# Optimization experiments

Hardware: AMD Instinct MI355X
Metric: run time of the kernel (lower is better)

Reference implementation:

```python
import jax, jax.numpy as jnp
import numpy as np

B, N, HID, H, DH, NB = 4, 4096, 768, 12, 64, 266
EPS = 1e-4


def softmax_kernel(data, proj, is_query):
    # data: [B,H,N,DH], proj: [NB,DH]. FAVOR+ positive softmax features.
    d = data.shape[-1]
    ratio = proj.shape[0] ** -0.5
    dn = d ** -0.25  # data normalizer
    data_dash = jnp.einsum('bhnd,jd->bhnj', data * dn, proj)  # [B,H,N,NB]
    diag = 0.5 * jnp.sum((data * dn) ** 2, axis=-1, keepdims=True)  # [B,H,N,1]
    if is_query:
        m = jnp.max(data_dash, axis=-1, keepdims=True)
    else:
        m = jnp.max(data_dash, axis=(-1, -2), keepdims=True)
    return ratio * (jnp.exp(data_dash - diag - m) + EPS)


def setup_inputs() -> dict:
    key = jax.random.key(0)
    ks = jax.random.split(key, 8)
    s = HID ** -0.5
    return {
        'hidden_states': jax.random.normal(ks[0], (B, N, HID), jnp.float32),
        'Wq': jax.random.normal(ks[1], (HID, HID), jnp.float32) * s,
        'bq': jnp.zeros((HID,), jnp.float32),
        'Wk': jax.random.normal(ks[2], (HID, HID), jnp.float32) * s,
        'bk': jnp.zeros((HID,), jnp.float32),
        'Wv': jax.random.normal(ks[3], (HID, HID), jnp.float32) * s,
        'bv': jnp.zeros((HID,), jnp.float32),
        'proj': jax.random.normal(ks[4], (NB, DH), jnp.float32),
    }


def reference(hidden_states, Wq, bq, Wk, bk, Wv, bv, proj):
    def heads(x):  # [B,N,HID] -> [B,H,N,DH]
        return x.reshape(B, N, H, DH).transpose(0, 2, 1, 3)

    q = heads(hidden_states @ Wq.T + bq)
    k = heads(hidden_states @ Wk.T + bk)
    v = heads(hidden_states @ Wv.T + bv)

    qp = softmax_kernel(q, proj, True)   # [B,H,N,NB]
    kp = softmax_kernel(k, proj, False)  # [B,H,N,NB]

    # non-causal linear attention: out = q' (k'^T v) / (q' sum_n k')
    k_sum = jnp.sum(kp, axis=2)                               # [B,H,NB]
    d_inv = 1.0 / jnp.einsum('bhnj,bhj->bhn', qp, k_sum)      # [B,H,N]
    ctx = jnp.einsum('bhnj,bhnd->bhjd', kp, v)                # [B,H,NB,DH]
    out = jnp.einsum('bhnj,bhjd->bhnd', qp, ctx) * d_inv[..., None]

    return out.transpose(0, 2, 1, 3).reshape(B, N, HID)
```

## Files before the change

kernel.cpp:

```cpp
#include <hip/hip_runtime.h>
#include <hip/hip_bf16.h>
#include <stdint.h>

#define B_   4
#define N_   4096
#define HID_ 768
#define H_   12
#define DH_  64
#define NB_  266
#define NBP_ 288
#define EPS_ 1e-4f
#define RATIO_ 0.06131393f

typedef unsigned short u16;
typedef __attribute__((ext_vector_type(8))) short short8;
typedef __attribute__((ext_vector_type(4))) float floatx4;

__device__ __forceinline__ u16 f2b(float f) {
  __hip_bfloat16 h = __float2bfloat16(f);
  return *reinterpret_cast<u16*>(&h);
}
__device__ __forceinline__ float b2f(u16 u) {
  union { unsigned u; float f; } x; x.u = ((unsigned)u) << 16; return x.f;
}
__device__ __forceinline__ unsigned fmap(float x) {
  unsigned u = __float_as_uint(x);
  return (u & 0x80000000u) ? ~u : (u | 0x80000000u);
}
__device__ __forceinline__ float funmap(unsigned u) {
  unsigned b = (u & 0x80000000u) ? (u & 0x7FFFFFFFu) : ~u;
  return __uint_as_float(b);
}
__device__ __forceinline__ void gl16(const u16* g, u16* l) {
  __builtin_amdgcn_global_load_lds(
      (const __attribute__((address_space(1))) void*)g,
      (__attribute__((address_space(3))) void*)l, 16, 0, 0);
}

__global__ __launch_bounds__(256) void k_prep(
    const float4* __restrict__ hs, const float4* __restrict__ Wq,
    const float4* __restrict__ Wk, const float4* __restrict__ Wv,
    const float* __restrict__ proj,
    uint2* __restrict__ hsb, uint2* __restrict__ wb3, u16* __restrict__ projb,
    unsigned* __restrict__ mbuf) {
  int blk = blockIdx.x;
  const int t = threadIdx.x;
  if (blk < 12288) {
    int i = blk * 256 + t;
    float4 v = hs[i];
    union { u16 s[4]; uint2 u; } pk;
    pk.s[0] = f2b(v.x); pk.s[1] = f2b(v.y); pk.s[2] = f2b(v.z); pk.s[3] = f2b(v.w);
    hsb[i] = pk.u;
    return;
  }
  blk -= 12288;
  if (blk < 1728) {
    int i = blk * 256 + t;
    int sel = i / 147456, j = i - sel * 147456;
    const float4* s = (sel == 0) ? Wq : (sel == 1) ? Wk : Wv;
    float4 v = s[j];
    union { u16 s4[4]; uint2 u; } pk;
    pk.s4[0] = f2b(v.x); pk.s4[1] = f2b(v.y); pk.s4[2] = f2b(v.z); pk.s4[3] = f2b(v.w);
    wb3[i] = pk.u;
    return;
  }
  blk -= 1728;
  if (blk < 72) {
    int i = blk * 256 + t;
    int j = i / DH_, d = i - j * DH_;
    float v = (j < NB_) ? proj[j * DH_ + d] * 0.35355339059327373f : 0.f;
    projb[i] = f2b(v);
    return;
  }
  blk -= 72;
  if (blk == 0 && t < B_ * H_) mbuf[t] = 0u;
}

__global__ __launch_bounds__(512, 2) void k_qkv2(
    const u16* __restrict__ hsb, const u16* __restrict__ wb,
    const float* __restrict__ bq, const float* __restrict__ bk, const float* __restrict__ bv,
    u16* __restrict__ qb, u16* __restrict__ kb, u16* __restrict__ vT) {
  __shared__ u16 lds[3 * 16384];
  const int orig = blockIdx.x;
  const int lg = (orig & 7) * 72 + (orig >> 3);
  const int tm = lg / 9, tn = lg - tm * 9;
  const int m0 = tm * 256;
  const int c0 = tn * 256;
  const int sel = c0 / 768;
  const int or0 = c0 - sel * 768;
  const u16* W = wb + (size_t)sel * HID_ * HID_;
  const int t = threadIdx.x, lane = t & 63, wv = t >> 6;
  const int lm = lane & 15, lq = lane >> 4;
  const int wvm = wv >> 2, wvn = wv & 3;
  const int srow = t >> 2;
  const int scol = ((t & 3) ^ ((t >> 3) & 3)) * 8;
  const u16* gA0 = hsb + (size_t)(m0 + srow) * HID_ + scol;
  const u16* gB0 = W + (size_t)(or0 + srow) * HID_ + scol;
  u16* lb = lds + wv * 512;
  const int slotc = (lq ^ ((lm >> 1) & 3)) * 8;
  const int aoff = (wvm * 128 + lm) * 32 + slotc;
  const int boff = 8192 + (wvn * 64 + lm) * 32 + slotc;

  floatx4 acc[8][4];
#pragma unroll
  for (int mt = 0; mt < 8; mt++)
#pragma unroll
    for (int nt = 0; nt < 4; nt++) acc[mt][nt] = (floatx4){0.f, 0.f, 0.f, 0.f};

#define STAGE_QKV(kt)                                            \
  {                                                              \
    const int k0_ = (kt) * 32;                                   \
    u16* l_ = lb + ((kt) % 3) * 16384;                           \
    gl16(gA0 + k0_, l_);                                         \
    gl16(gA0 + 128 * HID_ + k0_, l_ + 4096);                     \
    gl16(gB0 + k0_, l_ + 8192);                                  \
    gl16(gB0 + 128 * HID_ + k0_, l_ + 12288);                    \
  }

  STAGE_QKV(0);
  STAGE_QKV(1);
  asm volatile("s_waitcnt vmcnt(4)" ::: "memory");
  __builtin_amdgcn_s_barrier();

  for (int kt = 0; kt < 24; ++kt) {
    if (kt + 2 < 24) STAGE_QKV(kt + 2);
    const u16* bufA = lds + (kt % 3) * 16384;
    short8 af[8], bf[4];
#pragma unroll
    for (int mt = 0; mt < 8; mt++) af[mt] = *(const short8*)&bufA[aoff + mt * 512];
#pragma unroll
    for (int nt = 0; nt < 4; nt++) bf[nt] = *(const short8*)&bufA[boff + nt * 512];
    __builtin_amdgcn_s_setprio(1);
#pragma unroll
    for (int mt = 0; mt < 8; mt++)
#pragma unroll
      for (int nt = 0; nt < 4; nt++)
        acc[mt][nt] = __builtin_amdgcn_mfma_f32_16x16x32_bf16(af[mt], bf[nt], acc[mt][nt], 0, 0, 0);
    __builtin_amdgcn_s_setprio(0);
    if (kt < 22) asm volatile("s_waitcnt vmcnt(4)" ::: "memory");
    else         asm volatile("s_waitcnt vmcnt(0)" ::: "memory");
    __builtin_amdgcn_s_barrier();
  }
#undef STAGE_QKV

  if (sel < 2) {
    const float* bias = (sel == 0) ? bq : bk;
    u16* dst = (sel == 0) ? qb : kb;
#pragma unroll
    for (int nt = 0; nt < 4; nt++) {
      int lc = or0 + wvn * 64 + nt * 16 + lm;
      float bb = bias[lc];
#pragma unroll
      for (int mt = 0; mt < 8; mt++) {
        int rowb = m0 + wvm * 128 + mt * 16 + lq * 4;
#pragma unroll
        for (int r = 0; r < 4; r++)
          dst[(size_t)(rowb + r) * HID_ + lc] = f2b(acc[mt][nt][r] + bb);
      }
    }
  } else {
#pragma unroll
    for (int nt = 0; nt < 4; nt++) {
      int lc = or0 + wvn * 64 + nt * 16 + lm;
      int hh = lc >> 6, dv = lc & 63;
      float bb = bv[lc];
#pragma unroll
      for (int mt = 0; mt < 8; mt++) {
        int rowbase = m0 + wvm * 128 + mt * 16 + lq * 4;
        int b = rowbase >> 12, n = rowbase & 4095;
        union { u16 s[4]; uint2 u; } pk;
#pragma unroll
        for (int r = 0; r < 4; r++) pk.s[r] = f2b(acc[mt][nt][r] + bb);
        *(uint2*)(vT + ((size_t)(b * H_ + hh) * DH_ + dv) * N_ + n) = pk.u;
      }
    }
  }
}

__global__ __launch_bounds__(256) void k_kmax3(
    const u16* __restrict__ kb, const u16* __restrict__ projb,
    unsigned* __restrict__ mbuf, float* __restrict__ diagk) {
  const int bh = blockIdx.y, b = bh / H_, h = bh - b * H_;
  const int n0 = blockIdx.x * 256;
  const int t = threadIdx.x, lane = t & 63, wv = t >> 6;
  const int lm = lane & 15, lq = lane >> 4;
  const u16* kbase = kb + (size_t)(b * N_ + n0 + wv * 64) * HID_ + h * DH_;
  short8 af0[4], af1[4];
#pragma unroll
  for (int mt = 0; mt < 4; mt++) {
    const u16* p = kbase + (size_t)(mt * 16 + lm) * HID_ + lq * 8;
    af0[mt] = *(const short8*)p;
    af1[mt] = *(const short8*)(p + 32);
  }
#pragma unroll
  for (int mt = 0; mt < 4; mt++) {
    float rs = 0.f;
#pragma unroll
    for (int i = 0; i < 8; i++) { float f = b2f(((const u16*)&af0[mt])[i]); rs += f * f; }
#pragma unroll
    for (int i = 0; i < 8; i++) { float f = b2f(((const u16*)&af1[mt])[i]); rs += f * f; }
    rs += __shfl_xor(rs, 16);
    rs += __shfl_xor(rs, 32);
    if (lq == 0) diagk[(size_t)bh * N_ + n0 + wv * 64 + mt * 16 + lm] = 0.0625f * rs;
  }
  float mx = -3e38f;
  for (int ct = 0; ct < 17; ct++) {
    const u16* pp = projb + (ct * 16 + lm) * DH_ + lq * 8;
    short8 bf0 = *(const short8*)pp;
    short8 bf1 = *(const short8*)(pp + 32);
    bool valid = (ct < 16) || (lm < 10);
#pragma unroll
    for (int mt = 0; mt < 4; mt++) {
      floatx4 a = __builtin_amdgcn_mfma_f32_16x16x32_bf16(af0[mt], bf0, (floatx4){0.f,0.f,0.f,0.f}, 0, 0, 0);
      a = __builtin_amdgcn_mfma_f32_16x16x32_bf16(af1[mt], bf1, a, 0, 0, 0);
      if (valid) {
#pragma unroll
        for (int r = 0; r < 4; r++) mx = fmaxf(mx, a[r]);
      }
    }
  }
#pragma unroll
  for (int o = 1; o < 64; o <<= 1) mx = fmaxf(mx, __shfl_xor(mx, o));
  if (lane == 0) atomicMax(&mbuf[bh], fmap(mx));
}

__global__ __launch_bounds__(256) void k_ctx4(
    const u16* __restrict__ kb, const u16* __restrict__ vT, const u16* __restrict__ projb,
    const unsigned* __restrict__ mbuf, const float* __restrict__ diagk,
    float* __restrict__ ksum, u16* __restrict__ ctxb) {
  __shared__ u16 kpl[32 * 72];
  __shared__ float kred[4][2][16];
  const int orig = blockIdx.x;
  const int lg = (orig & 7) * 54 + (orig >> 3);
  const int bh = lg / 9, jb = lg - bh * 9;
  const int j0 = jb * 32;
  const int b = bh / H_, h = bh - b * H_;
  const int t = threadIdx.x, lane = t & 63, wv = t >> 6;
  const int lm = lane & 15, lq = lane >> 4;
  const float m = funmap(mbuf[bh]);
  const bool vj0 = (j0 + lm) < NB_;
  const bool vj1 = (j0 + 16 + lm) < NB_;
  short8 bp00, bp01, bp10, bp11;
  {
    const u16* pp = projb + (j0 + lm) * DH_ + lq * 8;
    bp00 = *(const short8*)pp;
    bp01 = *(const short8*)(pp + 32);
    pp += 16 * DH_;
    bp10 = *(const short8*)pp;
    bp11 = *(const short8*)(pp + 32);
  }
  const u16* kbB = kb + (size_t)(b * N_) * HID_ + h * DH_;
  const u16* vTb = vT + ((size_t)bh * DH_ + wv * 16 + lm) * N_;
  const float* dgB = diagk + (size_t)bh * N_;
  floatx4 acc0 = (floatx4){0.f,0.f,0.f,0.f}, acc1 = (floatx4){0.f,0.f,0.f,0.f};
  float kacc0 = 0.f, kacc1 = 0.f;
  const u16* kr0 = kbB + (size_t)(wv * 16 + lm) * HID_ + lq * 8;
  short8 af0 = *(const short8*)kr0;
  short8 af1 = *(const short8*)(kr0 + 32);
  floatx4 dg4 = *(const floatx4*)(dgB + wv * 16 + lq * 4);

  for (int n64 = 0; n64 < N_; n64 += 64) {
    __syncthreads();
    const int nn = (n64 + 64 < N_) ? n64 + 64 : 0;
    const u16* krn = kbB + (size_t)(nn + wv * 16 + lm) * HID_ + lq * 8;
    short8 nf0 = *(const short8*)krn;
    short8 nf1 = *(const short8*)(krn + 32);
    floatx4 nd = *(const floatx4*)(dgB + nn + wv * 16 + lq * 4);
    short8 av0 = *(const short8*)(vTb + n64 + lq * 8);
    short8 av1 = *(const short8*)(vTb + n64 + 32 + lq * 8);
    {
      floatx4 a = __builtin_amdgcn_mfma_f32_16x16x32_bf16(af0, bp00, (floatx4){0.f,0.f,0.f,0.f}, 0, 0, 0);
      a = __builtin_amdgcn_mfma_f32_16x16x32_bf16(af1, bp01, a, 0, 0, 0);
      union { u16 s[4]; uint2 u; } pk;
      float kss = 0.f;
#pragma unroll
      for (int r = 0; r < 4; r++) {
        float val = vj0 ? RATIO_ * (__expf(a[r] - dg4[r] - m) + EPS_) : 0.f;
        kss += val;
        pk.s[r] = f2b(val);
      }
      kacc0 += kss;
      *(uint2*)&kpl[lm * 72 + wv * 16 + lq * 4] = pk.u;
      a = __builtin_amdgcn_mfma_f32_16x16x32_bf16(af0, bp10, (floatx4){0.f,0.f,0.f,0.f}, 0, 0, 0);
      a = __builtin_amdgcn_mfma_f32_16x16x32_bf16(af1, bp11, a, 0, 0, 0);
      kss = 0.f;
#pragma unroll
      for (int r = 0; r < 4; r++) {
        float val = vj1 ? RATIO_ * (__expf(a[r] - dg4[r] - m) + EPS_) : 0.f;
        kss += val;
        pk.s[r] = f2b(val);
      }
      kacc1 += kss;
      *(uint2*)&kpl[(16 + lm) * 72 + wv * 16 + lq * 4] = pk.u;
    }
    __syncthreads();
    {
      short8 bf = *(const short8*)&kpl[lm * 72 + lq * 8];
      acc0 = __builtin_amdgcn_mfma_f32_16x16x32_bf16(av0, bf, acc0, 0, 0, 0);
      bf = *(const short8*)&kpl[(16 + lm) * 72 + lq * 8];
      acc1 = __builtin_amdgcn_mfma_f32_16x16x32_bf16(av0, bf, acc1, 0, 0, 0);
      bf = *(const short8*)&kpl[lm * 72 + 32 + lq * 8];
      acc0 = __builtin_amdgcn_mfma_f32_16x16x32_bf16(av1, bf, acc0, 0, 0, 0);
      bf = *(const short8*)&kpl[(16 + lm) * 72 + 32 + lq * 8];
      acc1 = __builtin_amdgcn_mfma_f32_16x16x32_bf16(av1, bf, acc1, 0, 0, 0);
    }
    af0 = nf0; af1 = nf1; dg4 = nd;
  }
  {
    float v0 = kacc0; v0 += __shfl_xor(v0, 16); v0 += __shfl_xor(v0, 32);
    float v1 = kacc1; v1 += __shfl_xor(v1, 16); v1 += __shfl_xor(v1, 32);
    if (lq == 0) { kred[wv][0][lm] = v0; kred[wv][1][lm] = v1; }
  }
  __syncthreads();
  if (t < 32) {
    int jh = t >> 4, l = t & 15;
    ksum[bh * NBP_ + j0 + t] =
        kred[0][jh][l] + kred[1][jh][l] + kred[2][jh][l] + kred[3][jh][l];
  }
  {
    u16* cb = ctxb + ((size_t)bh * DH_ + wv * 16 + lq * 4) * NBP_ + j0 + lm;
#pragma unroll
    for (int r = 0; r < 4; r++) {
      cb[(size_t)r * NBP_] = f2b(acc0[r]);
      cb[(size_t)r * NBP_ + 16] = f2b(acc1[r]);
    }
  }
}

__global__ __launch_bounds__(256) void k_out4(
    const u16* __restrict__ qb, const u16* __restrict__ projb,
    const u16* __restrict__ ctxb, const float* __restrict__ ksum,
    float* __restrict__ outp) {
  __shared__ u16 qpl[4][16][296];
  const int bh = blockIdx.y, b = bh / H_, h = bh - b * H_;
  const int t = threadIdx.x, lane = t & 63, wv = t >> 6;
  const int lm = lane & 15, lq = lane >> 4;
  const int row0 = blockIdx.x * 64 + wv * 16;
  const u16* cb = ctxb + (size_t)bh * DH_ * NBP_;
  const float* ksb = ksum + bh * NBP_;
  float ksv[17];
#pragma unroll
  for (int ct = 0; ct < 17; ct++) ksv[ct] = ksb[ct * 16 + lm];

  const u16* prow = qb + (size_t)(b * N_ + row0 + lm) * HID_ + h * DH_ + lq * 8;
  short8 af0 = *(const short8*)prow;
  short8 af1 = *(const short8*)(prow + 32);
  float rs = 0.f;
#pragma unroll
  for (int i = 0; i < 8; i++) { float f = b2f(((const u16*)&af0)[i]); rs += f * f; }
#pragma unroll
  for (int i = 0; i < 8; i++) { float f = b2f(((const u16*)&af1)[i]); rs += f * f; }
  rs += __shfl_xor(rs, 16);
  rs += __shfl_xor(rs, 32);
  float dg[4];
#pragma unroll
  for (int r = 0; r < 4; r++) dg[r] = 0.0625f * __shfl(rs, lq * 4 + r);

  floatx4 dd[17];
  float rm[4] = {-3e38f, -3e38f, -3e38f, -3e38f};
#pragma unroll
  for (int ct = 0; ct < 17; ct++) {
    const u16* pp = projb + (ct * 16 + lm) * DH_ + lq * 8;
    short8 bf0 = *(const short8*)pp;
    short8 bf1 = *(const short8*)(pp + 32);
    floatx4 a = __builtin_amdgcn_mfma_f32_16x16x32_bf16(af0, bf0, (floatx4){0.f,0.f,0.f,0.f}, 0, 0, 0);
    a = __builtin_amdgcn_mfma_f32_16x16x32_bf16(af1, bf1, a, 0, 0, 0);
    dd[ct] = a;
    if ((ct < 16) || (lm < 10)) {
#pragma unroll
      for (int r = 0; r < 4; r++) rm[r] = fmaxf(rm[r], a[r]);
    }
  }
#pragma unroll
  for (int o = 1; o < 16; o <<= 1) {
#pragma unroll
    for (int r = 0; r < 4; r++) rm[r] = fmaxf(rm[r], __shfl_xor(rm[r], o));
  }
  float dpart[4] = {0.f, 0.f, 0.f, 0.f};
#pragma unroll
  for (int ct = 0; ct < 17; ct++) {
    bool valid = (ct < 16) || (lm < 10);
#pragma unroll
    for (int r = 0; r < 4; r++) {
      float qpv = valid ? RATIO_ * (__expf(dd[ct][r] - dg[r] - rm[r]) + EPS_) : 0.f;
      dpart[r] += qpv * ksv[ct];
      qpl[wv][lq * 4 + r][ct * 16 + lm] = f2b(qpv);
    }
  }
#pragma unroll
  for (int r = 0; r < 4; r++) qpl[wv][lq * 4 + r][272 + lm] = 0;
#pragma unroll
  for (int o = 1; o < 16; o <<= 1) {
#pragma unroll
    for (int r = 0; r < 4; r++) dpart[r] += __shfl_xor(dpart[r], o);
  }
  float dinv[4];
#pragma unroll
  for (int r = 0; r < 4; r++) dinv[r] = 1.f / dpart[r];

  floatx4 ao[4];
#pragma unroll
  for (int dt = 0; dt < 4; dt++) ao[dt] = (floatx4){0.f, 0.f, 0.f, 0.f};
#pragma unroll
  for (int ks9 = 0; ks9 < 9; ks9++) {
    short8 aq = *(const short8*)&qpl[wv][lm][ks9 * 32 + lq * 8];
#pragma unroll
    for (int dt = 0; dt < 4; dt++) {
      short8 bc = *(const short8*)(cb + (size_t)(dt * 16 + lm) * NBP_ + ks9 * 32 + lq * 8);
      ao[dt] = __builtin_amdgcn_mfma_f32_16x16x32_bf16(aq, bc, ao[dt], 0, 0, 0);
    }
  }
#pragma unroll
  for (int dt = 0; dt < 4; dt++) {
#pragma unroll
    for (int r = 0; r < 4; r++) {
      int n = row0 + lq * 4 + r;
      outp[((size_t)(b * N_ + n)) * HID_ + h * DH_ + dt * 16 + lm] = ao[dt][r] * dinv[r];
    }
  }
}

extern "C" void kernel_launch(void* const* d_in, const int* in_sizes, int n_in,
                              void* d_out, int out_size, void* d_ws, size_t ws_size,
                              hipStream_t stream) {
  (void)in_sizes; (void)n_in; (void)out_size; (void)ws_size;
  const float* hs   = (const float*)d_in[0];
  const float* Wq   = (const float*)d_in[1];
  const float* bq   = (const float*)d_in[2];
  const float* Wk   = (const float*)d_in[3];
  const float* bk   = (const float*)d_in[4];
  const float* Wv   = (const float*)d_in[5];
  const float* bv   = (const float*)d_in[6];
  const float* proj = (const float*)d_in[7];

  char* w = (char*)d_ws;
  u16* hsb   = (u16*)w;  w += (size_t)16384 * 768 * 2;
  u16* wb3   = (u16*)w;  w += (size_t)3 * 768 * 768 * 2;
  u16* projb = (u16*)w;  w += (size_t)NBP_ * 64 * 2;
  u16* qb    = (u16*)w;  w += (size_t)16384 * 768 * 2;
  u16* kb    = (u16*)w;  w += (size_t)16384 * 768 * 2;
  u16* vT    = (u16*)w;  w += (size_t)48 * DH_ * N_ * 2;
  float* ksum  = (float*)w; w += (size_t)48 * NBP_ * 4;
  float* diagk = (float*)w; w += (size_t)48 * N_ * 4;
  u16* ctxTb = (u16*)w;  w += (size_t)48 * DH_ * NBP_ * 2;
  unsigned* mbuf = (unsigned*)w;

  hipLaunchKernelGGL(k_prep, dim3(14089), dim3(256), 0, stream,
                     (const float4*)hs, (const float4*)Wq, (const float4*)Wk, (const float4*)Wv,
                     proj, (uint2*)hsb, (uint2*)wb3, projb, mbuf);
  hipLaunchKernelGGL(k_qkv2, dim3(576), dim3(512), 0, stream, hsb, wb3, bq, bk, bv, qb, kb, vT);
  hipLaunchKernelGGL(k_kmax3, dim3(16, 48), dim3(256), 0, stream, kb, projb, mbuf, diagk);
  hipLaunchKernelGGL(k_ctx4, dim3(432), dim3(256), 0, stream, kb, vT, projb, mbuf, diagk, ksum, ctxTb);
  hipLaunchKernelGGL(k_out4, dim3(64, 48), dim3(256), 0, stream, qb, projb, ctxTb, ksum, (float*)d_out);
}
```

Baseline: 388.6 us.

## Fold global key max out of exp to remove separate k-max pass

Removes the k_kmax3 kernel, which recomputed the key projections only to find the global max. Key features are now computed without subtracting the max; the max is gathered during k_ctx5 and applied afterwards as a scale in a small finishing kernel. The EPS term's contribution is rebuilt from column sums of V, accumulated atomically in the QKV epilogue, and the per-row query max is handled algebraically in the output kernel. The key diagonal term also moves into the QKV epilogue. Costs are an extra tiny kernel, fp32 intermediates, and a risk of exp overflow without max subtraction.

```diff
diff --git a/kernel.cpp b/kernel.cpp
--- a/kernel.cpp
+++ b/kernel.cpp
@@ -42,7 +42,7 @@
     const float4* __restrict__ Wk, const float4* __restrict__ Wv,
     const float* __restrict__ proj,
     uint2* __restrict__ hsb, uint2* __restrict__ wb3, u16* __restrict__ projb,
-    unsigned* __restrict__ mbuf) {
+    float* __restrict__ Vdz, unsigned* __restrict__ mbuf) {
   int blk = blockIdx.x;
   const int t = threadIdx.x;
   if (blk < 12288) {
@@ -73,13 +73,19 @@
     return;
   }
   blk -= 72;
-  if (blk == 0 && t < B_ * H_) mbuf[t] = 0u;
+  if (blk < 12) {
+    int i = blk * 256 + t;
+    Vdz[i] = 0.f;
+    return;
+  }
+  if (t < B_ * H_) mbuf[t] = 0u;
 }
 
 __global__ __launch_bounds__(512, 2) void k_qkv2(
     const u16* __restrict__ hsb, const u16* __restrict__ wb,
     const float* __restrict__ bq, const float* __restrict__ bk, const float* __restrict__ bv,
-    u16* __restrict__ qb, u16* __restrict__ kb, u16* __restrict__ vT) {
+    u16* __restrict__ qb, u16* __restrict__ kb, u16* __restrict__ vT,
+    float* __restrict__ diagk, float* __restrict__ Vd) {
   __shared__ u16 lds[3 * 16384];
   const int orig = blockIdx.x;
   const int lg = (orig & 7) * 72 + (orig >> 3);
@@ -143,91 +149,85 @@
   }
 #undef STAGE_QKV
 
-  if (sel < 2) {
-    const float* bias = (sel == 0) ? bq : bk;
-    u16* dst = (sel == 0) ? qb : kb;
+  if (sel == 0) {
 #pragma unroll
     for (int nt = 0; nt < 4; nt++) {
       int lc = or0 + wvn * 64 + nt * 16 + lm;
-      float bb = bias[lc];
+      float bb = bq[lc];
 #pragma unroll
       for (int mt = 0; mt < 8; mt++) {
         int rowb = m0 + wvm * 128 + mt * 16 + lq * 4;
 #pragma unroll
         for (int r = 0; r < 4; r++)
-          dst[(size_t)(rowb + r) * HID_ + lc] = f2b(acc[mt][nt][r] + bb);
-      }
-    }
+          qb[(size_t)(rowb + r) * HID_ + lc] = f2b(acc[mt][nt][r] + bb);
+      }
+    }
+  } else if (sel == 1) {
+    float dsq[8][4];
+#pragma unroll
+    for (int mt = 0; mt < 8; mt++)
+#pragma unroll
+      for (int r = 0; r < 4; r++) dsq[mt][r] = 0.f;
+#pragma unroll
+    for (int nt = 0; nt < 4; nt++) {
+      int lc = or0 + wvn * 64 + nt * 16 + lm;
+      float bb = bk[lc];
+#pragma unroll
+      for (int mt = 0; mt < 8; mt++) {
+        int rowb = m0 + wvm * 128 + mt * 16 + lq * 4;
+#pragma unroll
+        for (int r = 0; r < 4; r++) {
+          u16 hv = f2b(acc[mt][nt][r] + bb);
+          kb[(size_t)(rowb + r) * HID_ + lc] = hv;
+          float fv = b2f(hv);
+          dsq[mt][r] += fv * fv;
+        }
+      }
+    }
+    const int bh0 = (m0 >> 12) * H_ + (or0 >> 6) + wvn;
+#pragma unroll
+    for (int mt = 0; mt < 8; mt++)
+#pragma unroll
+      for (int r = 0; r < 4; r++) {
+        float v = dsq[mt][r];
+        v += __shfl_xor(v, 1); v += __shfl_xor(v, 2);
+        v += __shfl_xor(v, 4); v += __shfl_xor(v, 8);
+        if (lm == 0) {
+          int rowb = m0 + wvm * 128 + mt * 16 + lq * 4 + r;
+          diagk[(size_t)bh0 * N_ + (rowb & 4095)] = 0.0625f * v;
+        }
+      }
   } else {
 #pragma unroll
     for (int nt = 0; nt < 4; nt++) {
       int lc = or0 + wvn * 64 + nt * 16 + lm;
       int hh = lc >> 6, dv = lc & 63;
       float bb = bv[lc];
+      float vs = 0.f;
 #pragma unroll
       for (int mt = 0; mt < 8; mt++) {
         int rowbase = m0 + wvm * 128 + mt * 16 + lq * 4;
         int b = rowbase >> 12, n = rowbase & 4095;
         union { u16 s[4]; uint2 u; } pk;
 #pragma unroll
-        for (int r = 0; r < 4; r++) pk.s[r] = f2b(acc[mt][nt][r] + bb);
+        for (int r = 0; r < 4; r++) {
+          float fv = acc[mt][nt][r] + bb;
+          vs += fv;
+          pk.s[r] = f2b(fv);
+        }
         *(uint2*)(vT + ((size_t)(b * H_ + hh) * DH_ + dv) * N_ + n) = pk.u;
       }
-    }
-  }
-}
-
-__global__ __launch_bounds__(256) void k_kmax3(
-    const u16* __restrict__ kb, const u16* __restrict__ projb,
-    unsigned* __restrict__ mbuf, float* __restrict__ diagk) {
-  const int bh = blockIdx.y, b = bh / H_, h = bh - b * H_;
-  const int n0 = blockIdx.x * 256;
-  const int t = threadIdx.x, lane = t & 63, wv = t >> 6;
-  const int lm = lane & 15, lq = lane >> 4;
-  const u16* kbase = kb + (size_t)(b * N_ + n0 + wv * 64) * HID_ + h * DH_;
-  short8 af0[4], af1[4];
-#pragma unroll
-  for (int mt = 0; mt < 4; mt++) {
-    const u16* p = kbase + (size_t)(mt * 16 + lm) * HID_ + lq * 8;
-    af0[mt] = *(const short8*)p;
-    af1[mt] = *(const short8*)(p + 32);
-  }
-#pragma unroll
-  for (int mt = 0; mt < 4; mt++) {
-    float rs = 0.f;
-#pragma unroll
-    for (int i = 0; i < 8; i++) { float f = b2f(((const u16*)&af0[mt])[i]); rs += f * f; }
-#pragma unroll
-    for (int i = 0; i < 8; i++) { float f = b2f(((const u16*)&af1[mt])[i]); rs += f * f; }
-    rs += __shfl_xor(rs, 16);
-    rs += __shfl_xor(rs, 32);
-    if (lq == 0) diagk[(size_t)bh * N_ + n0 + wv * 64 + mt * 16 + lm] = 0.0625f * rs;
-  }
-  float mx = -3e38f;
-  for (int ct = 0; ct < 17; ct++) {
-    const u16* pp = projb + (ct * 16 + lm) * DH_ + lq * 8;
-    short8 bf0 = *(const short8*)pp;
-    short8 bf1 = *(const short8*)(pp + 32);
-    bool valid = (ct < 16) || (lm < 10);
-#pragma unroll
-    for (int mt = 0; mt < 4; mt++) {
-      floatx4 a = __builtin_amdgcn_mfma_f32_16x16x32_bf16(af0[mt], bf0, (floatx4){0.f,0.f,0.f,0.f}, 0, 0, 0);
-      a = __builtin_amdgcn_mfma_f32_16x16x32_bf16(af1[mt], bf1, a, 0, 0, 0);
-      if (valid) {
-#pragma unroll
-        for (int r = 0; r < 4; r++) mx = fmaxf(mx, a[r]);
-      }
-    }
-  }
-#pragma unroll
-  for (int o = 1; o < 64; o <<= 1) mx = fmaxf(mx, __shfl_xor(mx, o));
-  if (lane == 0) atomicMax(&mbuf[bh], fmap(mx));
-}
-
-__global__ __launch_bounds__(256) void k_ctx4(
+      vs += __shfl_xor(vs, 16);
+      vs += __shfl_xor(vs, 32);
+      if (lq == 0) atomicAdd(&Vd[((m0 >> 12) * H_ + hh) * DH_ + dv], vs);
+    }
+  }
+}
+
+__global__ __launch_bounds__(256) void k_ctx5(
     const u16* __restrict__ kb, const u16* __restrict__ vT, const u16* __restrict__ projb,
-    const unsigned* __restrict__ mbuf, const float* __restrict__ diagk,
-    float* __restrict__ ksum, u16* __restrict__ ctxb) {
+    const float* __restrict__ diagk,
+    float* __restrict__ ksumS, float* __restrict__ ctxTf, unsigned* __restrict__ mbuf) {
   __shared__ u16 kpl[32 * 72];
   __shared__ float kred[4][2][16];
   const int orig = blockIdx.x;
@@ -237,7 +237,6 @@
   const int b = bh / H_, h = bh - b * H_;
   const int t = threadIdx.x, lane = t & 63, wv = t >> 6;
   const int lm = lane & 15, lq = lane >> 4;
-  const float m = funmap(mbuf[bh]);
   const bool vj0 = (j0 + lm) < NB_;
   const bool vj1 = (j0 + 16 + lm) < NB_;
   short8 bp00, bp01, bp10, bp11;
@@ -254,6 +253,7 @@
   const float* dgB = diagk + (size_t)bh * N_;
   floatx4 acc0 = (floatx4){0.f,0.f,0.f,0.f}, acc1 = (floatx4){0.f,0.f,0.f,0.f};
   float kacc0 = 0.f, kacc1 = 0.f;
+  float am = -3e38f;
   const u16* kr0 = kbB + (size_t)(wv * 16 + lm) * HID_ + lq * 8;
   short8 af0 = *(const short8*)kr0;
   short8 af1 = *(const short8*)(kr0 + 32);
@@ -275,9 +275,10 @@
       float kss = 0.f;
 #pragma unroll
       for (int r = 0; r < 4; r++) {
-        float val = vj0 ? RATIO_ * (__expf(a[r] - dg4[r] - m) + EPS_) : 0.f;
-        kss += val;
-        pk.s[r] = f2b(val);
+        float tv = __expf(a[r] - dg4[r]);
+        if (vj0) am = fmaxf(am, a[r]);
+        kss += tv;
+        pk.s[r] = f2b(tv);
       }
       kacc0 += kss;
       *(uint2*)&kpl[lm * 72 + wv * 16 + lq * 4] = pk.u;
@@ -286,9 +287,10 @@
       kss = 0.f;
 #pragma unroll
       for (int r = 0; r < 4; r++) {
-        float val = vj1 ? RATIO_ * (__expf(a[r] - dg4[r] - m) + EPS_) : 0.f;
-        kss += val;
-        pk.s[r] = f2b(val);
+        float tv = __expf(a[r] - dg4[r]);
+        if (vj1) am = fmaxf(am, a[r]);
+        kss += tv;
+        pk.s[r] = f2b(tv);
       }
       kacc1 += kss;
       *(uint2*)&kpl[(16 + lm) * 72 + wv * 16 + lq * 4] = pk.u;
@@ -314,22 +316,61 @@
   __syncthreads();
   if (t < 32) {
     int jh = t >> 4, l = t & 15;
-    ksum[bh * NBP_ + j0 + t] =
+    ksumS[bh * NBP_ + j0 + t] =
         kred[0][jh][l] + kred[1][jh][l] + kred[2][jh][l] + kred[3][jh][l];
   }
   {
-    u16* cb = ctxb + ((size_t)bh * DH_ + wv * 16 + lq * 4) * NBP_ + j0 + lm;
+    float* cb = ctxTf + ((size_t)bh * DH_ + wv * 16 + lq * 4) * NBP_ + j0 + lm;
 #pragma unroll
     for (int r = 0; r < 4; r++) {
-      cb[(size_t)r * NBP_] = f2b(acc0[r]);
-      cb[(size_t)r * NBP_ + 16] = f2b(acc1[r]);
-    }
-  }
-}
-
-__global__ __launch_bounds__(256) void k_out4(
+      cb[(size_t)r * NBP_] = acc0[r];
+      cb[(size_t)r * NBP_ + 16] = acc1[r];
+    }
+  }
+#pragma unroll
+  for (int o = 1; o < 64; o <<= 1) am = fmaxf(am, __shfl_xor(am, o));
+  if (lane == 0) atomicMax(&mbuf[bh], fmap(am));
+}
+
+__global__ __launch_bounds__(256) void k_fin(
+    const float* __restrict__ ctxTf, const float* __restrict__ ksumS,
+    const float* __restrict__ Vd, const unsigned* __restrict__ mbuf,
+    u16* __restrict__ ctxb, float* __restrict__ ksumf,
+    float* __restrict__ Cc, float* __restrict__ Ck) {
+  __shared__ float cks[4];
+  const int bh = blockIdx.x;
+  const int t = threadIdx.x;
+  const float em = __expf(-funmap(mbuf[bh]));
+  const int d = t >> 2, q4 = t & 3;
+  const float* Tb = ctxTf + ((size_t)bh * DH_ + d) * NBP_;
+  u16* cbo = ctxb + ((size_t)bh * DH_ + d) * NBP_;
+  const float vd = Vd[bh * DH_ + d];
+  float csum = 0.f;
+  for (int j = q4 * 72; j < q4 * 72 + 72; j++) {
+    float c = (j < NB_) ? RATIO_ * (em * Tb[j] + EPS_ * vd) : 0.f;
+    csum += c;
+    cbo[j] = f2b(c);
+  }
+  csum += __shfl_xor(csum, 1);
+  csum += __shfl_xor(csum, 2);
+  if (q4 == 0) Cc[bh * DH_ + d] = csum;
+  float ck = 0.f;
+  for (int j = t; j < NBP_; j += 256) {
+    float kv = (j < NB_) ? RATIO_ * (em * ksumS[bh * NBP_ + j] + EPS_ * 4096.0f) : 0.f;
+    ksumf[bh * NBP_ + j] = kv;
+    ck += kv;
+  }
+#pragma unroll
+  for (int o = 1; o < 64; o <<= 1) ck += __shfl_xor(ck, o);
+  if ((t & 63) == 0) cks[t >> 6] = ck;
+  __syncthreads();
+  if (t == 0) Ck[bh] = cks[0] + cks[1] + cks[2] + cks[3];
+}
+
+__global__ __launch_bounds__(256) void k_out5(
     const u16* __restrict__ qb, const u16* __restrict__ projb,
-    const u16* __restrict__ ctxb, const float* __restrict__ ksum,
+    const u16* __restrict__ ctxb, const float* __restrict__ ksumf,
+    const float* __restrict__ Cc, const float* __restrict__ Ck,
     float* __restrict__ outp) {
   __shared__ u16 qpl[4][16][296];
   const int bh = blockIdx.y, b = bh / H_, h = bh - b * H_;
@@ -337,10 +378,11 @@
   const int lm = lane & 15, lq = lane >> 4;
   const int row0 = blockIdx.x * 64 + wv * 16;
   const u16* cb = ctxb + (size_t)bh * DH_ * NBP_;
-  const float* ksb = ksum + bh * NBP_;
+  const float* ksb = ksumf + bh * NBP_;
   float ksv[17];
 #pragma unroll
   for (int ct = 0; ct < 17; ct++) ksv[ct] = ksb[ct * 16 + lm];
+  const float ckv = Ck[bh];
 
   const u16* prow = qb + (size_t)(b * N_ + row0 + lm) * HID_ + h * DH_ + lq * 8;
   short8 af0 = *(const short8*)prow;
@@ -356,8 +398,8 @@
 #pragma unroll
   for (int r = 0; r < 4; r++) dg[r] = 0.0625f * __shfl(rs, lq * 4 + r);
 
-  floatx4 dd[17];
-  float rm[4] = {-3e38f, -3e38f, -3e38f, -3e38f};
+  float tmax[4] = {0.f, 0.f, 0.f, 0.f};
+  float skp[4] = {0.f, 0.f, 0.f, 0.f};
 #pragma unroll
   for (int ct = 0; ct < 17; ct++) {
     const u16* pp = projb + (ct * 16 + lm) * DH_ + lq * 8;
@@ -365,38 +407,33 @@
     short8 bf1 = *(const short8*)(pp + 32);
     floatx4 a = __builtin_amdgcn_mfma_f32_16x16x32_bf16(af0, bf0, (floatx4){0.f,0.f,0.f,0.f}, 0, 0, 0);
     a = __builtin_amdgcn_mfma_f32_16x16x32_bf16(af1, bf1, a, 0, 0, 0);
-    dd[ct] = a;
-    if ((ct < 16) || (lm < 10)) {
-#pragma unroll
-      for (int r = 0; r < 4; r++) rm[r] = fmaxf(rm[r], a[r]);
-    }
-  }
+    bool valid = (ct < 16) || (lm < 10);
+#pragma unroll
+    for (int r = 0; r < 4; r++) {
+      float tv = __expf(a[r] - dg[r]);
+      if (valid) tmax[r] = fmaxf(tmax[r], tv);
+      skp[r] += tv * ksv[ct];
+      qpl[wv][lq * 4 + r][ct * 16 + lm] = f2b(tv);
+    }
+  }
+#pragma unroll
+  for (int r = 0; r < 4; r++) qpl[wv][lq * 4 + r][272 + lm] = 0;
 #pragma unroll
   for (int o = 1; o < 16; o <<= 1) {
 #pragma unroll
-    for (int r = 0; r < 4; r++) rm[r] = fmaxf(rm[r], __shfl_xor(rm[r], o));
-  }
-  float dpart[4] = {0.f, 0.f, 0.f, 0.f};
-#pragma unroll
-  for (int ct = 0; ct < 17; ct++) {
-    bool valid = (ct < 16) || (lm < 10);
-#pragma unroll
     for (int r = 0; r < 4; r++) {
-      float qpv = valid ? RATIO_ * (__expf(dd[ct][r] - dg[r] - rm[r]) + EPS_) : 0.f;
-      dpart[r] += qpv * ksv[ct];
-      qpl[wv][lq * 4 + r][ct * 16 + lm] = f2b(qpv);
-    }
-  }
-#pragma unroll
-  for (int r = 0; r < 4; r++) qpl[wv][lq * 4 + r][272 + lm] = 0;
-#pragma unroll
-  for (int o = 1; o < 16; o <<= 1) {
-#pragma unroll
-    for (int r = 0; r < 4; r++) dpart[r] += __shfl_xor(dpart[r], o);
-  }
-  float dinv[4];
-#pragma unroll
-  for (int r = 0; r < 4; r++) dinv[r] = 1.f / dpart[r];
+      tmax[r] = fmaxf(tmax[r], __shfl_xor(tmax[r], o));
+      skp[r] += __shfl_xor(skp[r], o);
+    }
+  }
+  float alpha[4], beta[4];
+#pragma unroll
+  for (int r = 0; r < 4; r++) {
+    float s = __expf(-dg[r]) / tmax[r];
+    float dinv = 1.f / (s * skp[r] + EPS_ * ckv);
+    alpha[r] = s * dinv;
+    beta[r] = EPS_ * dinv;
+  }
 
   floatx4 ao[4];
 #pragma unroll
@@ -412,10 +449,12 @@
   }
 #pragma unroll
   for (int dt = 0; dt < 4; dt++) {
+    float ccd = Cc[bh * DH_ + dt * 16 + lm];
 #pragma unroll
     for (int r = 0; r < 4; r++) {
       int n = row0 + lq * 4 + r;
-      outp[((size_t)(b * N_ + n)) * HID_ + h * DH_ + dt * 16 + lm] = ao[dt][r] * dinv[r];
+      outp[((size_t)(b * N_ + n)) * HID_ + h * DH_ + dt * 16 + lm] =
+          ao[dt][r] * alpha[r] + ccd * beta[r];
     }
   }
 }
@@ -440,16 +479,21 @@
   u16* qb    = (u16*)w;  w += (size_t)16384 * 768 * 2;
   u16* kb    = (u16*)w;  w += (size_t)16384 * 768 * 2;
   u16* vT    = (u16*)w;  w += (size_t)48 * DH_ * N_ * 2;
-  float* ksum  = (float*)w; w += (size_t)48 * NBP_ * 4;
+  float* ksumS = (float*)w; w += (size_t)48 * NBP_ * 4;
+  float* ksumf = (float*)w; w += (size_t)48 * NBP_ * 4;
   float* diagk = (float*)w; w += (size_t)48 * N_ * 4;
+  float* ctxTf = (float*)w; w += (size_t)48 * DH_ * NBP_ * 4;
   u16* ctxTb = (u16*)w;  w += (size_t)48 * DH_ * NBP_ * 2;
+  float* Vd   = (float*)w; w += (size_t)48 * DH_ * 4;
+  float* Cc   = (float*)w; w += (size_t)48 * DH_ * 4;
+  float* Ck   = (float*)w; w += (size_t)48 * 4;
   unsigned* mbuf = (unsigned*)w;
 
-  hipLaunchKernelGGL(k_prep, dim3(14089), dim3(256), 0, stream,
+  hipLaunchKernelGGL(k_prep, dim3(14101), dim3(256), 0, stream,
                      (const float4*)hs, (const float4*)Wq, (const float4*)Wk, (const float4*)Wv,
-                     proj, (uint2*)hsb, (uint2*)wb3, projb, mbuf);
-  hipLaunchKernelGGL(k_qkv2, dim3(576), dim3(512), 0, stream, hsb, wb3, bq, bk, bv, qb, kb, vT);
-  hipLaunchKernelGGL(k_kmax3, dim3(16, 48), dim3(256), 0, stream, kb, projb, mbuf, diagk);
-  hipLaunchKernelGGL(k_ctx4, dim3(432), dim3(256), 0, stream, kb, vT, projb, mbuf, diagk, ksum, ctxTb);
-  hipLaunchKernelGGL(k_out4, dim3(64, 48), dim3(256), 0, stream, qb, projb, ctxTb, ksum, (float*)d_out);
-}
+                     proj, (uint2*)hsb, (uint2*)wb3, projb, Vd, mbuf);
+  hipLaunchKernelGGL(k_qkv2, dim3(576), dim3(512), 0, stream, hsb, wb3, bq, bk, bv, qb, kb, vT, diagk, Vd);
+  hipLaunchKernelGGL(k_ctx5, dim3(432), dim3(256), 0, stream, kb, vT, projb, diagk, ksumS, ctxTf, mbuf);
+  hipLaunchKernelGGL(k_fin, dim3(48), dim3(256), 0, stream, ctxTf, ksumS, Vd, mbuf, ctxTb, ksumf, Cc, Ck);
+  hipLaunchKernelGGL(k_out5, dim3(64, 48), dim3(256), 0, stream, qb, projb, ctxTb, ksumf, Cc, Ck, (float*)d_out);
+}
```

Result: no change. 384.4 us (-1.1%).
